# Optimization experiments

Measured on AMD Instinct MI355X. Metric: run time of the kernel, lower is better.

Reference implementation:

```python
import jax, jax.numpy as jnp
import numpy as np

B, C, H, W = 32, 48, 64, 128
K = 5  # conv kernel size (1x5 / 5x1)


def _conv1d(x, w, b):
    # x: [B, C, L]; w: [O, I, K]; b: [O]. 'same' conv (pad 2) along L.
    y = jax.lax.conv_general_dilated(x, w, window_strides=(1,), padding=[(2, 2)],
                                     dimension_numbers=("NCH", "OIH", "NCH"))
    return y + b[None, :, None]


def setup_inputs() -> dict:
    key = jax.random.key(0)
    ks = jax.random.split(key, 7)
    s = 0.02  # small init so the 64/128-step linear recurrences stay bounded
    return {
        "x": jax.random.normal(ks[0], (B, C, H, W), dtype=jnp.float32),
        "down_w": jax.random.normal(ks[1], (C, C, K), dtype=jnp.float32) * s,
        "down_b": jax.random.normal(ks[2], (C,), dtype=jnp.float32) * s,
        "right_w": jax.random.normal(ks[3], (C, C, K), dtype=jnp.float32) * s,
        "right_b": jax.random.normal(ks[4], (C,), dtype=jnp.float32) * s,
        "left_w": jax.random.normal(ks[5], (C, C, K), dtype=jnp.float32) * s,
        "left_b": jax.random.normal(ks[6], (C,), dtype=jnp.float32) * s,
    }


def reference(x, down_w, down_b, right_w, right_b, left_w, left_b):
    Bb, Cc, Hh, Ww = x.shape

    def step(w, b):
        def f(carry, inp):
            nxt = inp + _conv1d(carry, w, b)
            return nxt, nxt
        return f

    # --- down pass: d[0]=x[0]; d[t]=x[t]+down_conv(d[t-1]) ---
    xs = jnp.moveaxis(x, 2, 0)                       # [H, B, C, W]
    d0 = xs[0]
    _, d_rest = jax.lax.scan(step(down_w, down_b), d0, xs[1:])
    D = jnp.concatenate([d0[None], d_rest], 0)       # [H, B, C, W]

    # --- up pass: faithfully uses down_conv (source quirk) with index H-3-t
    # u[0]=D[H-1]; u[k]=D[H-2-k]+down_conv(u[k-1]), k=1..H-1 (H-2-k=-1 -> D[H-1])
    seq = jnp.concatenate([D[Hh - 3::-1], D[Hh - 1:Hh]], 0)  # [H-1, B, C, W]
    u0 = D[Hh - 1]
    _, u_rest = jax.lax.scan(step(down_w, down_b), u0, seq)
    U = jnp.concatenate([u0[None], u_rest], 0)[::-1]  # U[i] = u[H-1-i]

    # --- right pass over width: r[0]=U[...,0]; r[t]=U[...,t]+right_conv(r[t-1]) ---
    ws = jnp.moveaxis(jnp.moveaxis(U, 0, 2), 3, 0)   # [W, B, C, H]
    r0 = ws[0]
    _, r_rest = jax.lax.scan(step(right_w, right_b), r0, ws[1:])
    R = jnp.concatenate([r0[None], r_rest], 0)       # [W, B, C, H]

    # --- left pass (reverse): l[0]=R[W-1]; l[k]=R[W-1-k]+left_conv(l[k-1]) ---
    l0 = R[Ww - 1]
    _, l_rest = jax.lax.scan(step(left_w, left_b), l0, R[Ww - 2::-1])
    L = jnp.concatenate([l0[None], l_rest], 0)[::-1]  # [W, B, C, H]

    return jnp.moveaxis(L, 0, 3)                     # [B, C, H, W]
```

## Files before the change

kernel.cpp:

```cpp
#include <hip/hip_runtime.h>
#include <hip/hip_bf16.h>

#define B_ 32
#define C_ 48
#define H_ 64
#define W_ 128
#define K_ 5
#define SLAB (C_*H_*W_)
#define RS 56
#define ROWS 136
#define CBUF (ROWS*RS)
#define WC (W_*C_)
#define HC (H_*C_)
#define KBN 8

typedef __attribute__((ext_vector_type(8))) short short8;
typedef __attribute__((ext_vector_type(4))) float f32x4;

__device__ __forceinline__ void lbar() {
  asm volatile("s_waitcnt lgkmcnt(0)\n\ts_barrier" ::: "memory");
}

__device__ __forceinline__ unsigned short f2bf(float f) {
  union { float f; unsigned u; } v; v.f = f;
  unsigned r = v.u + 0x7fffu + ((v.u >> 16) & 1u);
  return (unsigned short)(r >> 16);
}

__device__ __forceinline__ unsigned pk2(float a, float b) {
  union { __hip_bfloat162 h; unsigned u; } z;
  z.h = __float22bfloat162_rn(float2{a, b});
  return z.u;
}

__device__ __forceinline__ void load_wA(const float* __restrict__ wgt,
                                        const float* __restrict__ bias,
                                        short8 A[3][KBN], f32x4 bv[3],
                                        int l15, int q8, int c0) {
#pragma unroll
  for (int mt = 0; mt < 3; ++mt) {
#pragma unroll
    for (int r = 0; r < 4; ++r) bv[mt][r] = bias[mt * 16 + c0 + r];
#pragma unroll
    for (int kb = 0; kb < KBN; ++kb) {
      short8 f;
#pragma unroll
      for (int j = 0; j < 8; ++j) {
        int kp = kb * 32 + q8 + j;
        int k = kp / 48, i = kp - 48 * k;
        f[j] = (kp < 240)
             ? (short)f2bf(wgt[(mt * 16 + l15) * (C_ * K_) + i * K_ + k])
             : (short)0;
      }
      A[mt][kb] = f;
    }
  }
}

template<int NTW>
__device__ __forceinline__ void load_xin(float4 xv[NTW][3], const float* __restrict__ inp,
                                         size_t lRS, int n0, int l15, int c0) {
#pragma unroll
  for (int nt = 0; nt < NTW; ++nt) {
    const float* p = inp + (size_t)(n0 + nt * 16 + l15) * lRS + c0;
#pragma unroll
    for (int mt = 0; mt < 3; ++mt) xv[nt][mt] = *(const float4*)(p + mt * 16);
  }
}

template<int NTW, int SPL>
__device__ __forceinline__ void do_step(const unsigned short* __restrict__ scr,
                                        unsigned short* __restrict__ scw,
                                        const short8 A[3][KBN], const f32x4 bv[3],
                                        const float4 xv[NTW][3], const int off_r[KBN],
                                        float* __restrict__ outp,
                                        int n0, int l15, int c0) {
  f32x4 acc[SPL][NTW][3];
#pragma unroll
  for (int s = 0; s < SPL; ++s)
#pragma unroll
    for (int nt = 0; nt < NTW; ++nt)
#pragma unroll
      for (int mt = 0; mt < 3; ++mt)
        acc[s][nt][mt] = (s == 0) ? bv[mt] : (f32x4){0.f, 0.f, 0.f, 0.f};

#pragma unroll
  for (int kb = 0; kb < KBN; ++kb) {
    short8 pf[NTW];
#pragma unroll
    for (int nt = 0; nt < NTW; ++nt)
      pf[nt] = *(const short8*)(scr + (size_t)(n0 + nt * 16) * RS + off_r[kb]);
#pragma unroll
    for (int nt = 0; nt < NTW; ++nt)
#pragma unroll
      for (int mt = 0; mt < 3; ++mt)
        acc[kb % SPL][nt][mt] = __builtin_amdgcn_mfma_f32_16x16x32_bf16(
            A[mt][kb], pf[nt], acc[kb % SPL][nt][mt], 0, 0, 0);
  }

#pragma unroll
  for (int nt = 0; nt < NTW; ++nt) {
    const int row = n0 + nt * 16 + l15;
#pragma unroll
    for (int mt = 0; mt < 3; ++mt) {
      f32x4 a = acc[0][nt][mt];
#pragma unroll
      for (int s = 1; s < SPL; ++s)
#pragma unroll
        for (int r = 0; r < 4; ++r) a[r] += acc[s][nt][mt][r];
      float4 v;
      v.x = a[0] + xv[nt][mt].x; v.y = a[1] + xv[nt][mt].y;
      v.z = a[2] + xv[nt][mt].z; v.w = a[3] + xv[nt][mt].w;
      *(float4*)(outp + (size_t)row * C_ + mt * 16 + c0) = v;
      uint2 pk; pk.x = pk2(v.x, v.y); pk.y = pk2(v.z, v.w);
      *(uint2*)(scw + (size_t)(row + 2) * RS + mt * 16 + c0) = pk;
    }
  }
  lbar();
}

template<int NTW>
__device__ __forceinline__ void init_store(unsigned short* __restrict__ scw,
                                           const float* __restrict__ inp, size_t lRS,
                                           float* __restrict__ outp,
                                           int n0, int l15, int c0) {
  float4 xv[NTW][3];
  load_xin<NTW>(xv, inp, lRS, n0, l15, c0);
#pragma unroll
  for (int nt = 0; nt < NTW; ++nt) {
    const int row = n0 + nt * 16 + l15;
#pragma unroll
    for (int mt = 0; mt < 3; ++mt) {
      float4 v = xv[nt][mt];
      *(float4*)(outp + (size_t)row * C_ + mt * 16 + c0) = v;
      uint2 pk; pk.x = pk2(v.x, v.y); pk.y = pk2(v.z, v.w);
      *(uint2*)(scw + (size_t)(row + 2) * RS + mt * 16 + c0) = pk;
    }
  }
  lbar();
}

template<int NTW, int SPL, class FIN, class FOUT>
__device__ __forceinline__ void run_pass(unsigned short* sb, int& p,
                                         const short8 A[3][KBN], const f32x4 bv[3],
                                         const int off_r[KBN],
                                         int nsteps, FIN inadr, size_t lRS, FOUT outadr,
                                         int n0, int l15, int c0) {
  float4 xa[NTW][3], xb[NTW][3];
  load_xin<NTW>(xa, inadr(1), lRS, n0, l15, c0);
  for (int s = 1; s <= nsteps; s += 2) {
    {
      int sn = (s + 1 <= nsteps) ? s + 1 : nsteps;
      load_xin<NTW>(xb, inadr(sn), lRS, n0, l15, c0);
      __builtin_amdgcn_sched_barrier(0x38F);
      do_step<NTW, SPL>(sb + (size_t)p * CBUF, sb + (size_t)(p ^ 1) * CBUF,
                        A, bv, xa, off_r, outadr(s), n0, l15, c0);
      p ^= 1;
    }
    if (s + 1 <= nsteps) {
      int sn = (s + 2 <= nsteps) ? s + 2 : nsteps;
      load_xin<NTW>(xa, inadr(sn), lRS, n0, l15, c0);
      __builtin_amdgcn_sched_barrier(0x38F);
      do_step<NTW, SPL>(sb + (size_t)p * CBUF, sb + (size_t)(p ^ 1) * CBUF,
                        A, bv, xb, off_r, outadr(s + 1), n0, l15, c0);
      p ^= 1;
    }
  }
}

__global__ __launch_bounds__(256, 1) void scnn_mfma(
    float* ws,
    const float* __restrict__ dw, const float* __restrict__ db,
    const float* __restrict__ rw, const float* __restrict__ rb,
    const float* __restrict__ lw, const float* __restrict__ lb,
    float* __restrict__ DU)
{
  __shared__ unsigned short sb[2 * CBUF];
  const int tid = threadIdx.x, lane = tid & 63, wid = tid >> 6;
  const int l15 = lane & 15, q = lane >> 4, q8 = q * 8, c0 = 4 * q;
  const int b = blockIdx.x;
  float* xbuf = ws + (size_t)b * SLAB;
  float* rl   = ws + (size_t)b * SLAB;
  float* du   = DU + (size_t)b * SLAB;
  const int n0w = wid * 32, n0h = wid * 16;

  int off_r[KBN];
#pragma unroll
  for (int kb = 0; kb < KBN; ++kb) {
    int s = kb * 32 + q8;
    int k = s / 48, i0 = s - 48 * k;
    off_r[kb] = (l15 + k) * RS + i0;
  }

  short8 A[3][KBN];
  f32x4 bv[3];
  int p = 0;

  load_wA(dw, db, A, bv, l15, q8, c0);
  { unsigned* z = (unsigned*)sb; for (int i = tid; i < CBUF; i += 256) z[i] = 0u; }
  __syncthreads();
  init_store<2>(sb, xbuf, (size_t)C_, du, n0w, l15, c0);
  run_pass<2, 2>(sb, p, A, bv, off_r, H_ - 1,
                 [&](int s) { return xbuf + (size_t)s * WC; }, (size_t)C_,
                 [&](int s) { return du + (size_t)s * WC; }, n0w, l15, c0);
  __syncthreads();

  run_pass<2, 2>(sb, p, A, bv, off_r, H_ - 1,
                 [&](int s) { int ih = (s <= H_ - 2) ? (H_ - 2 - s) : (H_ - 1);
                              return du + (size_t)ih * WC; }, (size_t)C_,
                 [&](int s) { return du + (size_t)(H_ - 1 - s) * WC; }, n0w, l15, c0);
  __syncthreads();

  load_wA(rw, rb, A, bv, l15, q8, c0);
  { unsigned* z = (unsigned*)sb; for (int i = tid; i < CBUF; i += 256) z[i] = 0u; }
  __syncthreads();
  p = 0;
  init_store<1>(sb, du, (size_t)WC, rl, n0h, l15, c0);
  run_pass<1, 4>(sb, p, A, bv, off_r, W_ - 1,
                 [&](int s) { return du + (size_t)s * C_; }, (size_t)WC,
                 [&](int s) { return rl + (size_t)s * HC; }, n0h, l15, c0);
  __syncthreads();

  load_wA(lw, lb, A, bv, l15, q8, c0);
  run_pass<1, 4>(sb, p, A, bv, off_r, W_ - 1,
                 [&](int s) { return rl + (size_t)(W_ - 1 - s) * HC; }, (size_t)C_,
                 [&](int s) { return rl + (size_t)(W_ - 1 - s) * HC; }, n0h, l15, c0);
}

__global__ __launch_bounds__(256) void xpose_chw_hwc(const float* __restrict__ x,
                                                     float* __restrict__ xT) {
  __shared__ float t[C_ * 129];
  const int bh = blockIdx.x, b = bh >> 6, h = bh & 63;
  const float* src = x + (size_t)b * SLAB + (size_t)h * W_;
  float* dst = xT + (size_t)b * SLAB + (size_t)h * (W_ * C_);
  for (int i = threadIdx.x; i < C_ * W_; i += 256) {
    int c = i >> 7, w = i & 127;
    t[c * 129 + w] = src[(size_t)c * (H_ * W_) + w];
  }
  __syncthreads();
  for (int i = threadIdx.x; i < C_ * W_; i += 256) {
    int w = i / C_, c = i - w * C_;
    dst[i] = t[c * 129 + w];
  }
}

__global__ __launch_bounds__(256) void xpose_whc_chw(const float* __restrict__ L,
                                                     float* __restrict__ out) {
  __shared__ float t[W_ * 49];
  const int bh = blockIdx.x, b = bh >> 6, h = bh & 63;
  const float* src = L + (size_t)b * SLAB + (size_t)h * C_;
  float* dst = out + (size_t)b * SLAB + (size_t)h * W_;
  for (int i = threadIdx.x; i < W_ * C_; i += 256) {
    int w = i / C_, c = i - w * C_;
    t[w * 49 + c] = src[(size_t)w * (H_ * C_) + c];
  }
  __syncthreads();
  for (int i = threadIdx.x; i < C_ * W_; i += 256) {
    int c = i >> 7, w = i & 127;
    dst[(size_t)c * (H_ * W_) + w] = t[w * 49 + c];
  }
}

extern "C" void kernel_launch(void* const* d_in, const int* in_sizes, int n_in,
                              void* d_out, int out_size, void* d_ws, size_t ws_size,
                              hipStream_t stream) {
  const float* x  = (const float*)d_in[0];
  const float* dw = (const float*)d_in[1];
  const float* db = (const float*)d_in[2];
  const float* rw = (const float*)d_in[3];
  const float* rb = (const float*)d_in[4];
  const float* lw = (const float*)d_in[5];
  const float* lb = (const float*)d_in[6];
  float* DU = (float*)d_out;
  float* WS = (float*)d_ws;

  xpose_chw_hwc<<<B_ * H_, 256, 0, stream>>>(x, WS);
  scnn_mfma<<<B_, 256, 0, stream>>>(WS, dw, db, rw, rb, lw, lb, DU);
  xpose_whc_chw<<<B_ * H_, 256, 0, stream>>>(WS, DU);
}
```

Baseline: 408.8 us.

## Process two batch items per block to interleave independent recurrences

Each block now runs the recurrences of two batch elements side by side, so that the two independent MFMA chains and their LDS traffic can hide each other's latency within a single sequential step. The launch is halved to 16 blocks, and LDS now holds double buffers for both items. An XOR swizzle is added to the LDS row addressing to reduce bank conflicts. The software prefetch of the next step's inputs is removed, and the accumulator split is reduced. The risk is that only 16 of the many CUs stay busy and register pressure grows.

Result: slower. 1.097 ms (+168.4%).

```diff
diff --git a/kernel.cpp b/kernel.cpp
--- a/kernel.cpp
+++ b/kernel.cpp
@@ -8,14 +8,17 @@
 #define K_ 5
 #define SLAB (C_*H_*W_)
 #define RS 56
+#define RB 112
 #define ROWS 136
 #define CBUF (ROWS*RS)
+#define CBYTES (ROWS*RB)
 #define WC (W_*C_)
 #define HC (H_*C_)
 #define KBN 8
 
 typedef __attribute__((ext_vector_type(8))) short short8;
 typedef __attribute__((ext_vector_type(4))) float f32x4;
+typedef unsigned short ushort;
 
 __device__ __forceinline__ void lbar() {
   asm volatile("s_waitcnt lgkmcnt(0)\n\ts_barrier" ::: "memory");
@@ -35,7 +38,7 @@
 
 __device__ __forceinline__ void load_wA(const float* __restrict__ wgt,
                                         const float* __restrict__ bias,
-                                        short8 A[3][KBN], f32x4 bv[3],
+                                        short8 Aw[3][KBN], f32x4 bv[3],
                                         int l15, int q8, int c0) {
 #pragma unroll
   for (int mt = 0; mt < 3; ++mt) {
@@ -52,120 +55,131 @@
              ? (short)f2bf(wgt[(mt * 16 + l15) * (C_ * K_) + i * K_ + k])
              : (short)0;
       }
-      A[mt][kb] = f;
-    }
-  }
+      Aw[mt][kb] = f;
+    }
+  }
+}
+
+template<int NTW, int SPL>
+__device__ __forceinline__ void dual_step(
+    const char* __restrict__ scrA, char* __restrict__ scwA,
+    const char* __restrict__ scrB, char* __restrict__ scwB,
+    const short8 Aw[3][KBN], const f32x4 bv[3], const int offb[KBN],
+    const float* __restrict__ inA, const float* __restrict__ inB, size_t inRS,
+    float* __restrict__ outA, float* __restrict__ outB,
+    int n0, int l15, int c0, const int wcol[3])
+{
+  float4 xa[NTW][3], xb[NTW][3];
+#pragma unroll
+  for (int nt = 0; nt < NTW; ++nt) {
+    const float* pa = inA + (size_t)(n0 + nt * 16 + l15) * inRS + c0;
+    const float* pb = inB + (size_t)(n0 + nt * 16 + l15) * inRS + c0;
+#pragma unroll
+    for (int mt = 0; mt < 3; ++mt) {
+      xa[nt][mt] = *(const float4*)(pa + mt * 16);
+      xb[nt][mt] = *(const float4*)(pb + mt * 16);
+    }
+  }
+  __builtin_amdgcn_sched_barrier(0);
+
+  f32x4 acA[SPL][NTW][3], acB[SPL][NTW][3];
+#pragma unroll
+  for (int s = 0; s < SPL; ++s)
+#pragma unroll
+    for (int nt = 0; nt < NTW; ++nt)
+#pragma unroll
+      for (int mt = 0; mt < 3; ++mt) {
+        acA[s][nt][mt] = (s == 0) ? bv[mt] : (f32x4){0.f, 0.f, 0.f, 0.f};
+        acB[s][nt][mt] = (s == 0) ? bv[mt] : (f32x4){0.f, 0.f, 0.f, 0.f};
+      }
+
+  const char* bpA = scrA + (size_t)n0 * RB;
+  const char* bpB = scrB + (size_t)n0 * RB;
+#pragma unroll
+  for (int kb = 0; kb < KBN; ++kb) {
+    short8 pfa[NTW], pfb[NTW];
+#pragma unroll
+    for (int nt = 0; nt < NTW; ++nt) {
+      pfa[nt] = *(const short8*)(bpA + nt * (16 * RB) + offb[kb]);
+      pfb[nt] = *(const short8*)(bpB + nt * (16 * RB) + offb[kb]);
+    }
+#pragma unroll
+    for (int nt = 0; nt < NTW; ++nt)
+#pragma unroll
+      for (int mt = 0; mt < 3; ++mt) {
+        acA[kb % SPL][nt][mt] = __builtin_amdgcn_mfma_f32_16x16x32_bf16(
+            Aw[mt][kb], pfa[nt], acA[kb % SPL][nt][mt], 0, 0, 0);
+        acB[kb % SPL][nt][mt] = __builtin_amdgcn_mfma_f32_16x16x32_bf16(
+            Aw[mt][kb], pfb[nt], acB[kb % SPL][nt][mt], 0, 0, 0);
+      }
+  }
+
+#pragma unroll
+  for (int nt = 0; nt < NTW; ++nt) {
+    const int grow = n0 + nt * 16 + l15;
+    float* oa = outA + (size_t)grow * C_ + c0;
+    float* ob = outB + (size_t)grow * C_ + c0;
+    char* wa = scwA + (size_t)(grow + 2) * RB;
+    char* wb = scwB + (size_t)(grow + 2) * RB;
+#pragma unroll
+    for (int mt = 0; mt < 3; ++mt) {
+      f32x4 a = acA[0][nt][mt];
+#pragma unroll
+      for (int s = 1; s < SPL; ++s)
+#pragma unroll
+        for (int r = 0; r < 4; ++r) a[r] += acA[s][nt][mt][r];
+      float4 va;
+      va.x = a[0] + xa[nt][mt].x; va.y = a[1] + xa[nt][mt].y;
+      va.z = a[2] + xa[nt][mt].z; va.w = a[3] + xa[nt][mt].w;
+      *(float4*)(oa + mt * 16) = va;
+      uint2 pka; pka.x = pk2(va.x, va.y); pka.y = pk2(va.z, va.w);
+      *(uint2*)(wa + wcol[mt]) = pka;
+
+      f32x4 b2 = acB[0][nt][mt];
+#pragma unroll
+      for (int s = 1; s < SPL; ++s)
+#pragma unroll
+        for (int r = 0; r < 4; ++r) b2[r] += acB[s][nt][mt][r];
+      float4 vb;
+      vb.x = b2[0] + xb[nt][mt].x; vb.y = b2[1] + xb[nt][mt].y;
+      vb.z = b2[2] + xb[nt][mt].z; vb.w = b2[3] + xb[nt][mt].w;
+      *(float4*)(ob + mt * 16) = vb;
+      uint2 pkb; pkb.x = pk2(vb.x, vb.y); pkb.y = pk2(vb.z, vb.w);
+      *(uint2*)(wb + wcol[mt]) = pkb;
+    }
+  }
+  lbar();
 }
 
 template<int NTW>
-__device__ __forceinline__ void load_xin(float4 xv[NTW][3], const float* __restrict__ inp,
-                                         size_t lRS, int n0, int l15, int c0) {
+__device__ __forceinline__ void init_dual(
+    char* __restrict__ scwA, char* __restrict__ scwB,
+    const float* __restrict__ inA, const float* __restrict__ inB, size_t inRS,
+    float* __restrict__ outA, float* __restrict__ outB,
+    int n0, int l15, int c0, const int wcol[3])
+{
 #pragma unroll
   for (int nt = 0; nt < NTW; ++nt) {
-    const float* p = inp + (size_t)(n0 + nt * 16 + l15) * lRS + c0;
-#pragma unroll
-    for (int mt = 0; mt < 3; ++mt) xv[nt][mt] = *(const float4*)(p + mt * 16);
-  }
-}
-
-template<int NTW, int SPL>
-__device__ __forceinline__ void do_step(const unsigned short* __restrict__ scr,
-                                        unsigned short* __restrict__ scw,
-                                        const short8 A[3][KBN], const f32x4 bv[3],
-                                        const float4 xv[NTW][3], const int off_r[KBN],
-                                        float* __restrict__ outp,
-                                        int n0, int l15, int c0) {
-  f32x4 acc[SPL][NTW][3];
-#pragma unroll
-  for (int s = 0; s < SPL; ++s)
-#pragma unroll
-    for (int nt = 0; nt < NTW; ++nt)
-#pragma unroll
-      for (int mt = 0; mt < 3; ++mt)
-        acc[s][nt][mt] = (s == 0) ? bv[mt] : (f32x4){0.f, 0.f, 0.f, 0.f};
-
-#pragma unroll
-  for (int kb = 0; kb < KBN; ++kb) {
-    short8 pf[NTW];
-#pragma unroll
-    for (int nt = 0; nt < NTW; ++nt)
-      pf[nt] = *(const short8*)(scr + (size_t)(n0 + nt * 16) * RS + off_r[kb]);
-#pragma unroll
-    for (int nt = 0; nt < NTW; ++nt)
-#pragma unroll
-      for (int mt = 0; mt < 3; ++mt)
-        acc[kb % SPL][nt][mt] = __builtin_amdgcn_mfma_f32_16x16x32_bf16(
-            A[mt][kb], pf[nt], acc[kb % SPL][nt][mt], 0, 0, 0);
-  }
-
-#pragma unroll
-  for (int nt = 0; nt < NTW; ++nt) {
-    const int row = n0 + nt * 16 + l15;
+    const int grow = n0 + nt * 16 + l15;
+    const float* pa = inA + (size_t)grow * inRS + c0;
+    const float* pb = inB + (size_t)grow * inRS + c0;
+    float* oa = outA + (size_t)grow * C_ + c0;
+    float* ob = outB + (size_t)grow * C_ + c0;
+    char* wa = scwA + (size_t)(grow + 2) * RB;
+    char* wb = scwB + (size_t)(grow + 2) * RB;
 #pragma unroll
     for (int mt = 0; mt < 3; ++mt) {
-      f32x4 a = acc[0][nt][mt];
-#pragma unroll
-      for (int s = 1; s < SPL; ++s)
-#pragma unroll
-        for (int r = 0; r < 4; ++r) a[r] += acc[s][nt][mt][r];
-      float4 v;
-      v.x = a[0] + xv[nt][mt].x; v.y = a[1] + xv[nt][mt].y;
-      v.z = a[2] + xv[nt][mt].z; v.w = a[3] + xv[nt][mt].w;
-      *(float4*)(outp + (size_t)row * C_ + mt * 16 + c0) = v;
-      uint2 pk; pk.x = pk2(v.x, v.y); pk.y = pk2(v.z, v.w);
-      *(uint2*)(scw + (size_t)(row + 2) * RS + mt * 16 + c0) = pk;
+      float4 va = *(const float4*)(pa + mt * 16);
+      float4 vb = *(const float4*)(pb + mt * 16);
+      *(float4*)(oa + mt * 16) = va;
+      *(float4*)(ob + mt * 16) = vb;
+      uint2 pka; pka.x = pk2(va.x, va.y); pka.y = pk2(va.z, va.w);
+      uint2 pkb; pkb.x = pk2(vb.x, vb.y); pkb.y = pk2(vb.z, vb.w);
+      *(uint2*)(wa + wcol[mt]) = pka;
+      *(uint2*)(wb + wcol[mt]) = pkb;
     }
   }
   lbar();
-}
-
-template<int NTW>
-__device__ __forceinline__ void init_store(unsigned short* __restrict__ scw,
-                                           const float* __restrict__ inp, size_t lRS,
-                                           float* __restrict__ outp,
-                                           int n0, int l15, int c0) {
-  float4 xv[NTW][3];
-  load_xin<NTW>(xv, inp, lRS, n0, l15, c0);
-#pragma unroll
-  for (int nt = 0; nt < NTW; ++nt) {
-    const int row = n0 + nt * 16 + l15;
-#pragma unroll
-    for (int mt = 0; mt < 3; ++mt) {
-      float4 v = xv[nt][mt];
-      *(float4*)(outp + (size_t)row * C_ + mt * 16 + c0) = v;
-      uint2 pk; pk.x = pk2(v.x, v.y); pk.y = pk2(v.z, v.w);
-      *(uint2*)(scw + (size_t)(row + 2) * RS + mt * 16 + c0) = pk;
-    }
-  }
-  lbar();
-}
-
-template<int NTW, int SPL, class FIN, class FOUT>
-__device__ __forceinline__ void run_pass(unsigned short* sb, int& p,
-                                         const short8 A[3][KBN], const f32x4 bv[3],
-                                         const int off_r[KBN],
-                                         int nsteps, FIN inadr, size_t lRS, FOUT outadr,
-                                         int n0, int l15, int c0) {
-  float4 xa[NTW][3], xb[NTW][3];
-  load_xin<NTW>(xa, inadr(1), lRS, n0, l15, c0);
-  for (int s = 1; s <= nsteps; s += 2) {
-    {
-      int sn = (s + 1 <= nsteps) ? s + 1 : nsteps;
-      load_xin<NTW>(xb, inadr(sn), lRS, n0, l15, c0);
-      __builtin_amdgcn_sched_barrier(0x38F);
-      do_step<NTW, SPL>(sb + (size_t)p * CBUF, sb + (size_t)(p ^ 1) * CBUF,
-                        A, bv, xa, off_r, outadr(s), n0, l15, c0);
-      p ^= 1;
-    }
-    if (s + 1 <= nsteps) {
-      int sn = (s + 2 <= nsteps) ? s + 2 : nsteps;
-      load_xin<NTW>(xa, inadr(sn), lRS, n0, l15, c0);
-      __builtin_amdgcn_sched_barrier(0x38F);
-      do_step<NTW, SPL>(sb + (size_t)p * CBUF, sb + (size_t)(p ^ 1) * CBUF,
-                        A, bv, xb, off_r, outadr(s + 1), n0, l15, c0);
-      p ^= 1;
-    }
-  }
 }
 
 __global__ __launch_bounds__(256, 1) void scnn_mfma(
@@ -175,56 +189,85 @@
     const float* __restrict__ lw, const float* __restrict__ lb,
     float* __restrict__ DU)
 {
-  __shared__ unsigned short sb[2 * CBUF];
+  __shared__ __align__(32) ushort sball[2][2 * CBUF];
   const int tid = threadIdx.x, lane = tid & 63, wid = tid >> 6;
   const int l15 = lane & 15, q = lane >> 4, q8 = q * 8, c0 = 4 * q;
-  const int b = blockIdx.x;
-  float* xbuf = ws + (size_t)b * SLAB;
-  float* rl   = ws + (size_t)b * SLAB;
-  float* du   = DU + (size_t)b * SLAB;
+  const int bA = blockIdx.x * 2, bB = bA + 1;
+
+  float* xbufA = ws + (size_t)bA * SLAB;  float* xbufB = ws + (size_t)bB * SLAB;
+  float* rlA   = xbufA;                   float* rlB   = xbufB;
+  float* duA   = DU + (size_t)bA * SLAB;  float* duB   = DU + (size_t)bB * SLAB;
+  char* sbA = (char*)&sball[0][0];
+  char* sbB = (char*)&sball[1][0];
   const int n0w = wid * 32, n0h = wid * 16;
 
-  int off_r[KBN];
+  int offb[KBN];
 #pragma unroll
   for (int kb = 0; kb < KBN; ++kb) {
     int s = kb * 32 + q8;
     int k = s / 48, i0 = s - 48 * k;
-    off_r[kb] = (l15 + k) * RS + i0;
-  }
-
-  short8 A[3][KBN];
+    int e = l15 + k;
+    offb[kb] = e * RB + ((i0 * 2) ^ ((((e >> 3) & 1)) << 4));
+  }
+  const int wswz = (((l15 + 2) >> 3) & 1) << 4;
+  int wcol[3];
+#pragma unroll
+  for (int mt = 0; mt < 3; ++mt) wcol[mt] = mt * 32 + ((q * 8) ^ wswz);
+
+  short8 Aw[3][KBN];
   f32x4 bv[3];
   int p = 0;
 
-  load_wA(dw, db, A, bv, l15, q8, c0);
-  { unsigned* z = (unsigned*)sb; for (int i = tid; i < CBUF; i += 256) z[i] = 0u; }
-  __syncthreads();
-  init_store<2>(sb, xbuf, (size_t)C_, du, n0w, l15, c0);
-  run_pass<2, 2>(sb, p, A, bv, off_r, H_ - 1,
-                 [&](int s) { return xbuf + (size_t)s * WC; }, (size_t)C_,
-                 [&](int s) { return du + (size_t)s * WC; }, n0w, l15, c0);
-  __syncthreads();
-
-  run_pass<2, 2>(sb, p, A, bv, off_r, H_ - 1,
-                 [&](int s) { int ih = (s <= H_ - 2) ? (H_ - 2 - s) : (H_ - 1);
-                              return du + (size_t)ih * WC; }, (size_t)C_,
-                 [&](int s) { return du + (size_t)(H_ - 1 - s) * WC; }, n0w, l15, c0);
-  __syncthreads();
-
-  load_wA(rw, rb, A, bv, l15, q8, c0);
-  { unsigned* z = (unsigned*)sb; for (int i = tid; i < CBUF; i += 256) z[i] = 0u; }
+  load_wA(dw, db, Aw, bv, l15, q8, c0);
+  { unsigned* z = (unsigned*)&sball[0][0];
+    for (int i = tid; i < CBUF; i += 256) { z[i] = 0u; z[i + CBUF] = 0u; } }
+  __syncthreads();
+  init_dual<2>(sbA, sbB, xbufA, xbufB, (size_t)C_, duA, duB, n0w, l15, c0, wcol);
+  for (int s = 1; s < H_; ++s) {
+    dual_step<2, 1>(sbA + p * CBYTES, sbA + (p ^ 1) * CBYTES,
+                    sbB + p * CBYTES, sbB + (p ^ 1) * CBYTES, Aw, bv, offb,
+                    xbufA + (size_t)s * WC, xbufB + (size_t)s * WC, (size_t)C_,
+                    duA + (size_t)s * WC, duB + (size_t)s * WC, n0w, l15, c0, wcol);
+    p ^= 1;
+  }
+  __syncthreads();
+
+  for (int s = 1; s < H_; ++s) {
+    int ih = (s <= H_ - 2) ? (H_ - 2 - s) : (H_ - 1);
+    dual_step<2, 1>(sbA + p * CBYTES, sbA + (p ^ 1) * CBYTES,
+                    sbB + p * CBYTES, sbB + (p ^ 1) * CBYTES, Aw, bv, offb,
+                    duA + (size_t)ih * WC, duB + (size_t)ih * WC, (size_t)C_,
+                    duA + (size_t)(H_ - 1 - s) * WC, duB + (size_t)(H_ - 1 - s) * WC,
+                    n0w, l15, c0, wcol);
+    p ^= 1;
+  }
+  __syncthreads();
+
+  load_wA(rw, rb, Aw, bv, l15, q8, c0);
+  { unsigned* z = (unsigned*)&sball[0][0];
+    for (int i = tid; i < CBUF; i += 256) { z[i] = 0u; z[i + CBUF] = 0u; } }
   __syncthreads();
   p = 0;
-  init_store<1>(sb, du, (size_t)WC, rl, n0h, l15, c0);
-  run_pass<1, 4>(sb, p, A, bv, off_r, W_ - 1,
-                 [&](int s) { return du + (size_t)s * C_; }, (size_t)WC,
-                 [&](int s) { return rl + (size_t)s * HC; }, n0h, l15, c0);
-  __syncthreads();
-
-  load_wA(lw, lb, A, bv, l15, q8, c0);
-  run_pass<1, 4>(sb, p, A, bv, off_r, W_ - 1,
-                 [&](int s) { return rl + (size_t)(W_ - 1 - s) * HC; }, (size_t)C_,
-                 [&](int s) { return rl + (size_t)(W_ - 1 - s) * HC; }, n0h, l15, c0);
+  init_dual<1>(sbA, sbB, duA, duB, (size_t)WC, rlA, rlB, n0h, l15, c0, wcol);
+  for (int s = 1; s < W_; ++s) {
+    dual_step<1, 2>(sbA + p * CBYTES, sbA + (p ^ 1) * CBYTES,
+                    sbB + p * CBYTES, sbB + (p ^ 1) * CBYTES, Aw, bv, offb,
+                    duA + (size_t)s * C_, duB + (size_t)s * C_, (size_t)WC,
+                    rlA + (size_t)s * HC, rlB + (size_t)s * HC, n0h, l15, c0, wcol);
+    p ^= 1;
+  }
+  __syncthreads();
+
+  load_wA(lw, lb, Aw, bv, l15, q8, c0);
+  for (int s = 1; s < W_; ++s) {
+    dual_step<1, 2>(sbA + p * CBYTES, sbA + (p ^ 1) * CBYTES,
+                    sbB + p * CBYTES, sbB + (p ^ 1) * CBYTES, Aw, bv, offb,
+                    rlA + (size_t)(W_ - 1 - s) * HC, rlB + (size_t)(W_ - 1 - s) * HC,
+                    (size_t)C_,
+                    rlA + (size_t)(W_ - 1 - s) * HC, rlB + (size_t)(W_ - 1 - s) * HC,
+                    n0h, l15, c0, wcol);
+    p ^= 1;
+  }
 }
 
 __global__ __launch_bounds__(256) void xpose_chw_hwc(const float* __restrict__ x,
@@ -275,6 +318,6 @@
   float* WS = (float*)d_ws;
 
   xpose_chw_hwc<<<B_ * H_, 256, 0, stream>>>(x, WS);
-  scnn_mfma<<<B_, 256, 0, stream>>>(WS, dw, db, rw, rb, lw, lb, DU);
+  scnn_mfma<<<B_ / 2, 256, 0, stream>>>(WS, dw, db, rw, rb, lw, lb, DU);
   xpose_whc_chw<<<B_ * H_, 256, 0, stream>>>(WS, DU);
 }
```

## Pack two batch samples per 512-thread block and drop software prefetch of inputs

Applied to the files above, without the earlier changes.

The recurrence kernel now runs two independent batch samples per workgroup of 512 threads, each half using its own LDS double buffer, launching 16 blocks instead of 32. The explicit two-stage register prefetch of the next step's input is removed; inputs are loaded at the start of each step behind a sched barrier. The intent is to interleave two latency-bound recurrences on one CU so each hides the other's stalls, at the cost of using only half as many CUs and sharing block-wide barriers between the two samples.

Measured after the change: 887.9 us. +117.2%, slower.

```diff
diff --git a/kernel.cpp b/kernel.cpp
--- a/kernel.cpp
+++ b/kernel.cpp
@@ -16,6 +16,7 @@
 
 typedef __attribute__((ext_vector_type(8))) short short8;
 typedef __attribute__((ext_vector_type(4))) float f32x4;
+typedef unsigned short ushort;
 
 __device__ __forceinline__ void lbar() {
   asm volatile("s_waitcnt lgkmcnt(0)\n\ts_barrier" ::: "memory");
@@ -35,7 +36,7 @@
 
 __device__ __forceinline__ void load_wA(const float* __restrict__ wgt,
                                         const float* __restrict__ bias,
-                                        short8 A[3][KBN], f32x4 bv[3],
+                                        short8 Aw[3][KBN], f32x4 bv[3],
                                         int l15, int q8, int c0) {
 #pragma unroll
   for (int mt = 0; mt < 3; ++mt) {
@@ -52,29 +53,28 @@
              ? (short)f2bf(wgt[(mt * 16 + l15) * (C_ * K_) + i * K_ + k])
              : (short)0;
       }
-      A[mt][kb] = f;
+      Aw[mt][kb] = f;
     }
   }
 }
 
-template<int NTW>
-__device__ __forceinline__ void load_xin(float4 xv[NTW][3], const float* __restrict__ inp,
-                                         size_t lRS, int n0, int l15, int c0) {
-#pragma unroll
-  for (int nt = 0; nt < NTW; ++nt) {
-    const float* p = inp + (size_t)(n0 + nt * 16 + l15) * lRS + c0;
-#pragma unroll
-    for (int mt = 0; mt < 3; ++mt) xv[nt][mt] = *(const float4*)(p + mt * 16);
-  }
-}
-
 template<int NTW, int SPL>
-__device__ __forceinline__ void do_step(const unsigned short* __restrict__ scr,
-                                        unsigned short* __restrict__ scw,
-                                        const short8 A[3][KBN], const f32x4 bv[3],
-                                        const float4 xv[NTW][3], const int off_r[KBN],
+__device__ __forceinline__ void do_step(const ushort* __restrict__ scr,
+                                        ushort* __restrict__ scw,
+                                        const short8 Aw[3][KBN], const f32x4 bv[3],
+                                        const int off_r[KBN],
+                                        const float* __restrict__ inp, size_t inRS,
                                         float* __restrict__ outp,
                                         int n0, int l15, int c0) {
+  float4 xv[NTW][3];
+#pragma unroll
+  for (int nt = 0; nt < NTW; ++nt) {
+    const float* p = inp + (size_t)(n0 + nt * 16 + l15) * inRS + c0;
+#pragma unroll
+    for (int mt = 0; mt < 3; ++mt) xv[nt][mt] = *(const float4*)(p + mt * 16);
+  }
+  __builtin_amdgcn_sched_barrier(0);
+
   f32x4 acc[SPL][NTW][3];
 #pragma unroll
   for (int s = 0; s < SPL; ++s)
@@ -95,7 +95,7 @@
 #pragma unroll
       for (int mt = 0; mt < 3; ++mt)
         acc[kb % SPL][nt][mt] = __builtin_amdgcn_mfma_f32_16x16x32_bf16(
-            A[mt][kb], pf[nt], acc[kb % SPL][nt][mt], 0, 0, 0);
+            Aw[mt][kb], pf[nt], acc[kb % SPL][nt][mt], 0, 0, 0);
   }
 
 #pragma unroll
@@ -120,18 +120,17 @@
 }
 
 template<int NTW>
-__device__ __forceinline__ void init_store(unsigned short* __restrict__ scw,
-                                           const float* __restrict__ inp, size_t lRS,
+__device__ __forceinline__ void init_store(ushort* __restrict__ scw,
+                                           const float* __restrict__ inp, size_t inRS,
                                            float* __restrict__ outp,
                                            int n0, int l15, int c0) {
-  float4 xv[NTW][3];
-  load_xin<NTW>(xv, inp, lRS, n0, l15, c0);
 #pragma unroll
   for (int nt = 0; nt < NTW; ++nt) {
     const int row = n0 + nt * 16 + l15;
+    const float* p = inp + (size_t)row * inRS + c0;
 #pragma unroll
     for (int mt = 0; mt < 3; ++mt) {
-      float4 v = xv[nt][mt];
+      float4 v = *(const float4*)(p + mt * 16);
       *(float4*)(outp + (size_t)row * C_ + mt * 16 + c0) = v;
       uint2 pk; pk.x = pk2(v.x, v.y); pk.y = pk2(v.z, v.w);
       *(uint2*)(scw + (size_t)(row + 2) * RS + mt * 16 + c0) = pk;
@@ -141,47 +140,37 @@
 }
 
 template<int NTW, int SPL, class FIN, class FOUT>
-__device__ __forceinline__ void run_pass(unsigned short* sb, int& p,
-                                         const short8 A[3][KBN], const f32x4 bv[3],
+__device__ __forceinline__ void run_pass(ushort* sb, int& p,
+                                         const short8 Aw[3][KBN], const f32x4 bv[3],
                                          const int off_r[KBN],
-                                         int nsteps, FIN inadr, size_t lRS, FOUT outadr,
+                                         int nsteps, FIN inadr, size_t inRS, FOUT outadr,
                                          int n0, int l15, int c0) {
-  float4 xa[NTW][3], xb[NTW][3];
-  load_xin<NTW>(xa, inadr(1), lRS, n0, l15, c0);
-  for (int s = 1; s <= nsteps; s += 2) {
-    {
-      int sn = (s + 1 <= nsteps) ? s + 1 : nsteps;
-      load_xin<NTW>(xb, inadr(sn), lRS, n0, l15, c0);
-      __builtin_amdgcn_sched_barrier(0x38F);
-      do_step<NTW, SPL>(sb + (size_t)p * CBUF, sb + (size_t)(p ^ 1) * CBUF,
-                        A, bv, xa, off_r, outadr(s), n0, l15, c0);
-      p ^= 1;
-    }
-    if (s + 1 <= nsteps) {
-      int sn = (s + 2 <= nsteps) ? s + 2 : nsteps;
-      load_xin<NTW>(xa, inadr(sn), lRS, n0, l15, c0);
-      __builtin_amdgcn_sched_barrier(0x38F);
-      do_step<NTW, SPL>(sb + (size_t)p * CBUF, sb + (size_t)(p ^ 1) * CBUF,
-                        A, bv, xb, off_r, outadr(s + 1), n0, l15, c0);
-      p ^= 1;
-    }
-  }
-}
-
-__global__ __launch_bounds__(256, 1) void scnn_mfma(
+  for (int s = 1; s <= nsteps; ++s) {
+    do_step<NTW, SPL>(sb + (size_t)p * CBUF, sb + (size_t)(p ^ 1) * CBUF,
+                      Aw, bv, off_r, inadr(s), inRS, outadr(s), n0, l15, c0);
+    p ^= 1;
+  }
+}
+
+__global__ __attribute__((amdgpu_flat_work_group_size(512, 512),
+                          amdgpu_waves_per_eu(2, 2))) void scnn_mfma(
     float* ws,
     const float* __restrict__ dw, const float* __restrict__ db,
     const float* __restrict__ rw, const float* __restrict__ rb,
     const float* __restrict__ lw, const float* __restrict__ lb,
     float* __restrict__ DU)
 {
-  __shared__ unsigned short sb[2 * CBUF];
-  const int tid = threadIdx.x, lane = tid & 63, wid = tid >> 6;
+  __shared__ __align__(32) ushort sball[2][2 * CBUF];
+  const int tid = threadIdx.x;
+  const int sub = tid >> 8, t8 = tid & 255;
+  const int lane = tid & 63, wid = (tid >> 6) & 3;
   const int l15 = lane & 15, q = lane >> 4, q8 = q * 8, c0 = 4 * q;
-  const int b = blockIdx.x;
+  const int b = blockIdx.x * 2 + sub;
+
   float* xbuf = ws + (size_t)b * SLAB;
   float* rl   = ws + (size_t)b * SLAB;
   float* du   = DU + (size_t)b * SLAB;
+  ushort* sb  = &sball[sub][0];
   const int n0w = wid * 32, n0h = wid * 16;
 
   int off_r[KBN];
@@ -192,37 +181,37 @@
     off_r[kb] = (l15 + k) * RS + i0;
   }
 
-  short8 A[3][KBN];
+  short8 Aw[3][KBN];
   f32x4 bv[3];
   int p = 0;
 
-  load_wA(dw, db, A, bv, l15, q8, c0);
-  { unsigned* z = (unsigned*)sb; for (int i = tid; i < CBUF; i += 256) z[i] = 0u; }
+  load_wA(dw, db, Aw, bv, l15, q8, c0);
+  { unsigned* z = (unsigned*)sb; for (int i = t8; i < CBUF; i += 256) z[i] = 0u; }
   __syncthreads();
   init_store<2>(sb, xbuf, (size_t)C_, du, n0w, l15, c0);
-  run_pass<2, 2>(sb, p, A, bv, off_r, H_ - 1,
+  run_pass<2, 2>(sb, p, Aw, bv, off_r, H_ - 1,
                  [&](int s) { return xbuf + (size_t)s * WC; }, (size_t)C_,
                  [&](int s) { return du + (size_t)s * WC; }, n0w, l15, c0);
   __syncthreads();
 
-  run_pass<2, 2>(sb, p, A, bv, off_r, H_ - 1,
+  run_pass<2, 2>(sb, p, Aw, bv, off_r, H_ - 1,
                  [&](int s) { int ih = (s <= H_ - 2) ? (H_ - 2 - s) : (H_ - 1);
                               return du + (size_t)ih * WC; }, (size_t)C_,
                  [&](int s) { return du + (size_t)(H_ - 1 - s) * WC; }, n0w, l15, c0);
   __syncthreads();
 
-  load_wA(rw, rb, A, bv, l15, q8, c0);
-  { unsigned* z = (unsigned*)sb; for (int i = tid; i < CBUF; i += 256) z[i] = 0u; }
+  load_wA(rw, rb, Aw, bv, l15, q8, c0);
+  { unsigned* z = (unsigned*)sb; for (int i = t8; i < CBUF; i += 256) z[i] = 0u; }
   __syncthreads();
   p = 0;
   init_store<1>(sb, du, (size_t)WC, rl, n0h, l15, c0);
-  run_pass<1, 4>(sb, p, A, bv, off_r, W_ - 1,
+  run_pass<1, 4>(sb, p, Aw, bv, off_r, W_ - 1,
                  [&](int s) { return du + (size_t)s * C_; }, (size_t)WC,
                  [&](int s) { return rl + (size_t)s * HC; }, n0h, l15, c0);
   __syncthreads();
 
-  load_wA(lw, lb, A, bv, l15, q8, c0);
-  run_pass<1, 4>(sb, p, A, bv, off_r, W_ - 1,
+  load_wA(lw, lb, Aw, bv, l15, q8, c0);
+  run_pass<1, 4>(sb, p, Aw, bv, off_r, W_ - 1,
                  [&](int s) { return rl + (size_t)(W_ - 1 - s) * HC; }, (size_t)C_,
                  [&](int s) { return rl + (size_t)(W_ - 1 - s) * HC; }, n0h, l15, c0);
 }
@@ -275,6 +264,6 @@
   float* WS = (float*)d_ws;
 
   xpose_chw_hwc<<<B_ * H_, 256, 0, stream>>>(x, WS);
-  scnn_mfma<<<B_, 256, 0, stream>>>(WS, dw, db, rw, rb, lw, lb, DU);
+  scnn_mfma<<<B_ / 2, 512, 0, stream>>>(WS, dw, db, rw, rb, lw, lb, DU);
   xpose_whc_chw<<<B_ * H_, 256, 0, stream>>>(WS, DU);
 }
```
